# Kernel tuning notes

Measured on AMD Instinct MI355X. Metric: run time of the kernel, lower is better.

Reference implementation:

```python
import jax, jax.numpy as jnp
import numpy as np

B, C, H, W = 2, 256, 64, 64
KEEP = 0.1


def setup_inputs() -> dict:
    key = jax.random.key(0)
    ks = jax.random.split(key, 7)
    s = 0.05  # small init for 1x1-conv weights
    return {
        "x": jax.random.normal(ks[0], (B, C, H, W), dtype=jnp.float32),
        "Wq": jax.random.normal(ks[1], (C, C), dtype=jnp.float32) * s,
        "bq": jax.random.normal(ks[2], (C,), dtype=jnp.float32) * s,
        "Wk": jax.random.normal(ks[3], (C, C), dtype=jnp.float32) * s,
        "bk": jax.random.normal(ks[4], (C,), dtype=jnp.float32) * s,
        "Wv": jax.random.normal(ks[5], (C, C), dtype=jnp.float32) * s,
        "bv": jax.random.normal(ks[6], (C,), dtype=jnp.float32) * s,
    }


def reference(x, Wq, bq, Wk, bk, Wv, bv):
    b, c, h, w = x.shape
    n = h * w

    def proj(Wm, bm):
        # 1x1 conv == per-pixel linear; output as [B, N, C] tokens
        return jnp.einsum('bchw,oc->bhwo', x, Wm).reshape(b, n, c) + bm

    q = proj(Wq, bq)
    k = proj(Wk, bk)
    v = proj(Wv, bv)

    scores = jnp.einsum('bnc,bmc->bnm', q, k) / (c ** 0.5)  # [B, N, N]
    k_keep = max(1, int(KEEP * n))

    vals, idx = jax.lax.top_k(scores, k_keep)  # [B, N, k_keep]
    # softmax over -inf-masked scores == softmax over topk vals scattered into zeros
    probs = jax.nn.softmax(vals, axis=-1)
    attn = jnp.zeros_like(scores).at[
        jnp.arange(b)[:, None, None], jnp.arange(n)[None, :, None], idx
    ].set(probs)

    out = jnp.einsum('bnm,bmc->bnc', attn, v)  # [B, N, C]
    return out.transpose(0, 2, 1).reshape(b, c, h, w)
```

## Files before the change

kernel.cpp:

```cpp
#include <hip/hip_runtime.h>
#include <hip/hip_bf16.h>
#include <math.h>

#define BATCH 2
#define CC    256
#define NN    4096
#define KK    409
#define KCAT  768
#define SCALE 0.0625f
#define PSTRIDE 8192

typedef _Float16 half8 __attribute__((ext_vector_type(8)));
typedef float    floatx4 __attribute__((ext_vector_type(4)));

typedef __attribute__((address_space(3))) unsigned       lds_u32;
typedef __attribute__((address_space(1))) const unsigned glb_u32;
__device__ __forceinline__ void gload16(const void* g, void* l) {
    __builtin_amdgcn_global_load_lds((glb_u32*)g, (lds_u32*)l, 16, 0, 0);
}

__device__ __forceinline__ unsigned fkey(float f) {
    unsigned u = __float_as_uint(f);
    return (u & 0x80000000u) ? ~u : (u | 0x80000000u);
}
__device__ __forceinline__ float keyToF(unsigned k) {
    unsigned u = (k & 0x80000000u) ? (k ^ 0x80000000u) : ~k;
    return __uint_as_float(u);
}

__global__ __launch_bounds__(256) void xpose_wcat_kernel(
        const float* __restrict__ x,
        const float* __restrict__ Wq, const float* __restrict__ Wk,
        const float* __restrict__ Wv,
        _Float16* __restrict__ xcat, _Float16* __restrict__ Wcat) {
    const int t  = threadIdx.x;
    if (blockIdx.y == 4) {
        int idx = (blockIdx.z * 64 + blockIdx.x) * 256 + t;
#pragma unroll
        for (int k = 0; k < 6; k++) {
            int e = idx + k * 32768;
            int mat = e >> 16;
            int o   = (e >> 8) & 255;
            int c   = e & 255;
            const float* W = (mat == 0) ? Wq : (mat == 1) ? Wk : Wv;
            float v = W[o * 256 + c];
            _Float16 hi = (_Float16)v;
            _Float16 lo = (_Float16)(v - (float)hi);
            _Float16* wr = Wcat + ((size_t)(mat * 256 + o)) * KCAT;
            wr[c] = hi; wr[256 + c] = hi; wr[512 + c] = lo;
        }
        return;
    }

    __shared__ float xs[64][68];
    const int n0 = blockIdx.x * 64;
    const int c0 = blockIdx.y * 64;
    const int b  = blockIdx.z;

    {
        const int ci = t >> 2;
        const int j  = (t & 3) * 16;
        const float* xp = x + ((size_t)((b << 8) + c0 + ci)) * NN + n0 + j;
        float4 a0 = ((const float4*)xp)[0];
        float4 a1 = ((const float4*)xp)[1];
        float4 a2 = ((const float4*)xp)[2];
        float4 a3 = ((const float4*)xp)[3];
        *(float4*)&xs[ci][j]      = a0;
        *(float4*)&xs[ci][j + 4]  = a1;
        *(float4*)&xs[ci][j + 8]  = a2;
        *(float4*)&xs[ci][j + 12] = a3;
    }
    __syncthreads();

    const int n = t >> 2;
    const int g0 = t & 3;
    _Float16* xr = xcat + ((size_t)(b * NN + n0 + n)) * KCAT + c0;
#pragma unroll
    for (int gg = 0; gg < 2; gg++) {
        int g = g0 + gg * 4;
        half8 hi, lo;
#pragma unroll
        for (int k = 0; k < 8; k++) {
            float v = xs[g * 8 + k][n];
            _Float16 h = (_Float16)v;
            hi[k] = h;
            lo[k] = (_Float16)(v - (float)h);
        }
        *(half8*)(xr + g * 8)       = hi;
        *(half8*)(xr + 256 + g * 8) = lo;
        *(half8*)(xr + 512 + g * 8) = hi;
    }
}

__global__ __launch_bounds__(256) void proj_gemm(
        const _Float16* __restrict__ xcat, const _Float16* __restrict__ Wcat,
        const float* __restrict__ bq, const float* __restrict__ bk,
        const float* __restrict__ bv,
        _Float16* __restrict__ Qcat, _Float16* __restrict__ Kcat,
        _Float16* __restrict__ Vt) {
    __shared__ _Float16 As[128][64];
    __shared__ _Float16 Bs[128][64];

    const int t    = threadIdx.x;
    const int wave = t >> 6;
    const int l    = t & 63;
    const int wr   = wave >> 1;
    const int wc   = wave & 1;
    const int mat  = blockIdx.z;

    int bym, bxn;
    if (mat < 2) { bym = blockIdx.x >> 1; bxn = blockIdx.x & 1; }
    else         { bym = blockIdx.x & 1;  bxn = blockIdx.x >> 1; }

    const int lr = l >> 3;
    const int gg = (l & 7) ^ lr;

    const _Float16* At;
    const _Float16* Bt;
    if (mat < 2) {
        At = xcat + ((size_t)(bym * 128)) * KCAT;
        Bt = Wcat + ((size_t)(mat * 256 + bxn * 128)) * KCAT;
    } else {
        At = Wcat + ((size_t)(512 + bym * 128)) * KCAT;
        Bt = xcat + ((size_t)(bxn * 128)) * KCAT;
    }
    const size_t lane_off = (size_t)lr * KCAT + gg * 8;

    floatx4 acc[4][4];
#pragma unroll
    for (int i = 0; i < 4; i++)
#pragma unroll
        for (int j = 0; j < 4; j++) acc[i][j] = (floatx4)0.0f;

    const int rowA = l & 15;
    const int sg0  = (l >> 4) ^ (l & 7);
    const int sg1  = sg0 ^ 4;

    for (int kc = 0; kc < KCAT; kc += 64) {
#pragma unroll
        for (int s = 0; s < 4; s++) {
            const int seg = wave * 4 + s;
            gload16(At + (size_t)seg * 8 * KCAT + lane_off + kc, &As[seg * 8][0]);
            gload16(Bt + (size_t)seg * 8 * KCAT + lane_off + kc, &Bs[seg * 8][0]);
        }
        __syncthreads();
#pragma unroll
        for (int ks = 0; ks < 2; ks++) {
            const int sg = ks ? sg1 : sg0;
            half8 af[4], bf[4];
#pragma unroll
            for (int mi = 0; mi < 4; mi++)
                af[mi] = *(const half8*)&As[wr * 64 + mi * 16 + rowA][sg * 8];
#pragma unroll
            for (int ni = 0; ni < 4; ni++)
                bf[ni] = *(const half8*)&Bs[wc * 64 + ni * 16 + rowA][sg * 8];
#pragma unroll
            for (int mi = 0; mi < 4; mi++)
#pragma unroll
                for (int ni = 0; ni < 4; ni++)
                    acc[mi][ni] = __builtin_amdgcn_mfma_f32_16x16x32_f16(
                        af[mi], bf[ni], acc[mi][ni], 0, 0, 0);
        }
        __syncthreads();
    }

    if (mat < 2) {
        const float* bias = (mat == 0) ? bq : bk;
        _Float16* Out = (mat == 0) ? Qcat : Kcat;
#pragma unroll
        for (int ni = 0; ni < 4; ni++) {
            int ch = bxn * 128 + wc * 64 + ni * 16 + (l & 15);
            float bb = bias[ch];
#pragma unroll
            for (int mi = 0; mi < 4; mi++)
#pragma unroll
                for (int rg = 0; rg < 4; rg++) {
                    int token = bym * 128 + wr * 64 + mi * 16 + (l >> 4) * 4 + rg;
                    float v = acc[mi][ni][rg] + bb;
                    _Float16 hi = (_Float16)v;
                    _Float16 lo = (_Float16)(v - (float)hi);
                    _Float16* p = Out + (size_t)token * KCAT + ch;
                    if (mat == 0) { p[0] = hi; p[256] = lo; p[512] = hi; }
                    else          { p[0] = hi; p[256] = hi; p[512] = lo; }
                }
        }
    } else {
#pragma unroll
        for (int mi = 0; mi < 4; mi++)
#pragma unroll
            for (int rg = 0; rg < 4; rg++) {
                int ch = bym * 128 + wr * 64 + mi * 16 + (l >> 4) * 4 + rg;
                float bb = bv[ch];
#pragma unroll
                for (int ni = 0; ni < 4; ni++) {
                    int col = bxn * 128 + wc * 64 + ni * 16 + (l & 15);
                    int b = col >> 12, n = col & 4095;
                    Vt[((size_t)((b << 8) + ch)) * NN + n] =
                        (_Float16)(acc[mi][ni][rg] + bb);
                }
            }
    }
}

__global__ __launch_bounds__(512, 2) void score_gemm(
        const _Float16* __restrict__ Qcat, const _Float16* __restrict__ Kcat,
        float* __restrict__ S) {
    __shared__ _Float16 As[256][64];
    __shared__ _Float16 Bs[256][64];

    const int t    = threadIdx.x;
    const int wave = t >> 6;
    const int l    = t & 63;
    const int wr   = wave >> 1;
    const int wc   = wave & 1;

    const int id  = blockIdx.x;
    const int sc  = id & 7;
    const int j   = id >> 3;
    const int b   = sc & 1;
    const int scq = sc >> 1;
    const int bxn = ((scq & 1) << 3) + (j & 7);
    const int bym = ((scq >> 1) << 3) + (j >> 3);

    const int lr = l >> 3;
    const int gg = (l & 7) ^ lr;

    const _Float16* At = Qcat + ((size_t)((b << 12) + bym * 256)) * KCAT;
    const _Float16* Bt = Kcat + ((size_t)((b << 12) + bxn * 256)) * KCAT;
    const size_t lane_off = (size_t)lr * KCAT + gg * 8;

    floatx4 acc[4][8];
#pragma unroll
    for (int i = 0; i < 4; i++)
#pragma unroll
        for (int jj = 0; jj < 8; jj++) acc[i][jj] = (floatx4)0.0f;

    const int rowA = l & 15;
    const int sg0  = (l >> 4) ^ (l & 7);
    const int sg1  = sg0 ^ 4;

    for (int kc = 0; kc < KCAT; kc += 64) {
#pragma unroll
        for (int s = 0; s < 4; s++) {
            const int seg = wave * 4 + s;
            gload16(At + (size_t)seg * 8 * KCAT + lane_off + kc, &As[seg * 8][0]);
            gload16(Bt + (size_t)seg * 8 * KCAT + lane_off + kc, &Bs[seg * 8][0]);
        }
        __syncthreads();
#pragma unroll
        for (int ks = 0; ks < 2; ks++) {
            const int sg = ks ? sg1 : sg0;
            half8 af[4], bf[8];
#pragma unroll
            for (int mi = 0; mi < 4; mi++)
                af[mi] = *(const half8*)&As[wr * 64 + mi * 16 + rowA][sg * 8];
#pragma unroll
            for (int ni = 0; ni < 8; ni++)
                bf[ni] = *(const half8*)&Bs[wc * 128 + ni * 16 + rowA][sg * 8];
#pragma unroll
            for (int mi = 0; mi < 4; mi++)
#pragma unroll
                for (int ni = 0; ni < 8; ni++)
                    acc[mi][ni] = __builtin_amdgcn_mfma_f32_16x16x32_f16(
                        af[mi], bf[ni], acc[mi][ni], 0, 0, 0);
        }
        __syncthreads();
    }

    float* Sb = S + ((size_t)b << 24);
#pragma unroll
    for (int mi = 0; mi < 4; mi++)
#pragma unroll
        for (int ni = 0; ni < 8; ni++) {
            int col = bxn * 256 + wc * 128 + ni * 16 + (l & 15);
#pragma unroll
            for (int rg = 0; rg < 4; rg++) {
                int row = bym * 256 + wr * 64 + mi * 16 + (l >> 4) * 4 + rg;
                Sb[((size_t)row << 12) + col] = acc[mi][ni][rg] * SCALE;
            }
        }
}

__global__ __launch_bounds__(256) void select_scatter(
        const float* __restrict__ S, _Float16* __restrict__ P) {
    __shared__ unsigned hist[256];
    __shared__ unsigned scan[256];
    __shared__ unsigned candKey[NN];
    __shared__ unsigned wred[4];
    __shared__ float    fmn[4], fmx[4], wsum[4];
    __shared__ unsigned sh_d, sh_cntgt, sh_T;
    __shared__ int      sh_ncand, sh_need;

    const int t = threadIdx.x;
    const int l = t & 63;
    const int w = t >> 6;

    float    val[16];
    unsigned ukey[16];
    {
        const float*  Srow = S + ((size_t)blockIdx.x << 12);
        const float4* sp   = (const float4*)(Srow + t * 16);
#pragma unroll
        for (int jj = 0; jj < 4; jj++) {
            float4 v = sp[jj];
            val[jj * 4 + 0] = v.x; val[jj * 4 + 1] = v.y;
            val[jj * 4 + 2] = v.z; val[jj * 4 + 3] = v.w;
        }
#pragma unroll
        for (int j = 0; j < 16; j++) ukey[j] = fkey(val[j]);
    }

    float lmin = val[0], lmax = val[0];
#pragma unroll
    for (int j = 1; j < 16; j++) {
        lmin = fminf(lmin, val[j]); lmax = fmaxf(lmax, val[j]);
    }
#pragma unroll
    for (int off = 32; off > 0; off >>= 1) {
        float a = __shfl_down(lmin, off);
        float b = __shfl_down(lmax, off);
        if (l + off < 64) { lmin = fminf(lmin, a); lmax = fmaxf(lmax, b); }
    }
    if (l == 0) { fmn[w] = lmin; fmx[w] = lmax; }

    hist[t] = 0u;
    if (t == 0) sh_ncand = 0;
    __syncthreads();
    const float fmin = fminf(fminf(fmn[0], fmn[1]), fminf(fmn[2], fmn[3]));
    const float fmax = fmaxf(fmaxf(fmx[0], fmx[1]), fmaxf(fmx[2], fmx[3]));
    const float range = fmax - fmin;
    const float bscale = (range > 1e-20f) ? 255.0f / range : 0.0f;

    auto binOf = [&](float v) -> int {
        int bin = (int)((v - fmin) * bscale);
        return bin < 0 ? 0 : (bin > 255 ? 255 : bin);
    };

#pragma unroll
    for (int j = 0; j < 16; j++) atomicAdd(&hist[binOf(val[j])], 1u);
    __syncthreads();

    int rem = KK;

    auto find_digit = [&](int remv) {
        unsigned v = hist[t];
#pragma unroll
        for (int off = 1; off < 64; off <<= 1) {
            unsigned o = __shfl_down(v, off);
            if (l + off < 64) v += o;
        }
        if (l == 0) wred[w] = v;
        __syncthreads();
        unsigned add = 0u;
#pragma unroll
        for (int w2 = 0; w2 < 4; w2++) if (w2 > w) add += wred[w2];
        scan[t] = v + add;
        __syncthreads();
        unsigned sufd  = scan[t];
        unsigned sufd1 = (t < 255) ? scan[t + 1] : 0u;
        if (sufd >= (unsigned)remv && sufd1 < (unsigned)remv) {
            sh_d = (unsigned)t; sh_cntgt = sufd1;
        }
        __syncthreads();
    };

    find_digit(rem);
    const int dbin = (int)sh_d;
    rem -= (int)sh_cntgt;

#pragma unroll
    for (int j = 0; j < 16; j++) {
        if (binOf(val[j]) == dbin) {
            int slot = atomicAdd(&sh_ncand, 1);
            candKey[slot] = ukey[j];
        }
    }
    __syncthreads();
    const int nc = sh_ncand;

    if (nc <= 64) {
        if (w == 0) {
            unsigned kl = (l < nc) ? candKey[l] : 0u;
            int r = 0, g = 0;
            for (int j = 0; j < 64; j++) {
                unsigned kj = __shfl(kl, j);
                bool gt = kj > kl;
                g += gt ? 1 : 0;
                r += (gt || (kj == kl && j < l)) ? 1 : 0;
            }
            if (r == rem - 1) { sh_T = kl; sh_need = rem - g; }
        }
    } else {
        unsigned prefix = 0u;
        int rem2 = rem;
        for (int pass = 0; pass < 4; pass++) {
            const int shift = 24 - 8 * pass;
            hist[t] = 0u;
            __syncthreads();
            for (int i = t; i < nc; i += 256) {
                unsigned u2 = candKey[i];
                if (pass == 0 || (u2 >> (shift + 8)) == (prefix >> (shift + 8)))
                    atomicAdd(&hist[(u2 >> shift) & 255u], 1u);
            }
            __syncthreads();
            find_digit(rem2);
            prefix |= (sh_d << shift);
            rem2 -= (int)sh_cntgt;
        }
        if (t == 0) { sh_T = prefix; sh_need = rem2; }
    }
    __syncthreads();
    const unsigned T = sh_T;
    const int need = sh_need;
    const float mT = keyToF(T);

    int eqc = 0;
#pragma unroll
    for (int j = 0; j < 16; j++) if (ukey[j] == T) eqc++;
    int vinc = eqc;
#pragma unroll
    for (int off = 1; off < 64; off <<= 1) {
        int o = __shfl_up(vinc, off);
        if (l >= off) vinc += o;
    }
    if (l == 63) wred[w] = (unsigned)vinc;
    __syncthreads();
    int addlow = 0;
#pragma unroll
    for (int w2 = 0; w2 < 4; w2++) if (w2 < w) addlow += (int)wred[w2];
    const int eqexcl = vinc - eqc + addlow;

    float pv[16];
    float le = 0.f;
#pragma unroll
    for (int j = 0; j < 16; j++) {
        float e = 0.f;
        if (ukey[j] > T) { e = __expf(val[j] - mT); le += e; }
        pv[j] = e;
    }
    if (eqc) {
        int seen = 0;
#pragma unroll
        for (int j = 0; j < 16; j++) {
            if (ukey[j] == T) {
                if (eqexcl + seen < need) { pv[j] = 1.0f; le += 1.0f; }
                seen++;
            }
        }
    }

#pragma unroll
    for (int off = 32; off > 0; off >>= 1) {
        float o = __shfl_down(le, off);
        if (l + off < 64) le += o;
    }
    if (l == 0) wsum[w] = le;
    __syncthreads();
    const float inv = 1.0f / (wsum[0] + wsum[1] + wsum[2] + wsum[3]);

    half8 ra, rb;
#pragma unroll
    for (int j = 0; j < 8; j++) {
        ra[j] = (_Float16)(pv[j] * inv);
        rb[j] = (_Float16)(pv[j + 8] * inv);
    }
    _Float16* Pr = P + (size_t)blockIdx.x * PSTRIDE + t * 16;
    *(half8*)Pr       = ra;
    *(half8*)(Pr + 8) = rb;
}

__global__ __launch_bounds__(256) void av_gemm(
        const _Float16* __restrict__ Vt, const _Float16* __restrict__ P,
        float* __restrict__ out) {
    __shared__ _Float16 As0[64][64], As1[64][64];
    __shared__ _Float16 Bs0[64][64], Bs1[64][64];

    const int t    = threadIdx.x;
    const int wave = t >> 6;
    const int l    = t & 63;
    const int wr   = wave >> 1;
    const int wc   = wave & 1;
    const int bxn  = blockIdx.x;
    const int byc  = blockIdx.y;
    const int b    = blockIdx.z;

    const int lr = l >> 3;
    const int gg = (l & 7) ^ lr;

    const _Float16* At = Vt + ((size_t)((b << 8) + byc * 64)) * NN;
    const _Float16* Bt = P + ((size_t)(b * NN + bxn * 64)) * PSTRIDE;
    const size_t lane_offA = (size_t)lr * NN + gg * 8;
    const size_t lane_offB = (size_t)lr * PSTRIDE + gg * 8;

    floatx4 acc[2][2];
#pragma unroll
    for (int i = 0; i < 2; i++)
#pragma unroll
        for (int j = 0; j < 2; j++) acc[i][j] = (floatx4)0.0f;

    const int rowA   = l & 15;
    const int sgbase = (l >> 4) ^ (l & 7);

    for (int kc = 0; kc < NN; kc += 128) {
#pragma unroll
        for (int s = 0; s < 2; s++) {
            const int seg = wave * 2 + s;
            gload16(At + (size_t)seg * 8 * NN + lane_offA + kc,           &As0[seg * 8][0]);
            gload16(At + (size_t)seg * 8 * NN + lane_offA + kc + 64,      &As1[seg * 8][0]);
            gload16(Bt + (size_t)seg * 8 * PSTRIDE + lane_offB + kc,      &Bs0[seg * 8][0]);
            gload16(Bt + (size_t)seg * 8 * PSTRIDE + lane_offB + kc + 64, &Bs1[seg * 8][0]);
        }
        __syncthreads();
#pragma unroll
        for (int st = 0; st < 4; st++) {
            const _Float16 (*Ap)[64] = (st < 2) ? As0 : As1;
            const _Float16 (*Bp)[64] = (st < 2) ? Bs0 : Bs1;
            const int sg = sgbase ^ ((st & 1) ? 4 : 0);
            half8 af[2], bf[2];
#pragma unroll
            for (int mi = 0; mi < 2; mi++)
                af[mi] = *(const half8*)&Ap[wr * 32 + mi * 16 + rowA][sg * 8];
#pragma unroll
            for (int ni = 0; ni < 2; ni++)
                bf[ni] = *(const half8*)&Bp[wc * 32 + ni * 16 + rowA][sg * 8];
#pragma unroll
            for (int mi = 0; mi < 2; mi++)
#pragma unroll
                for (int ni = 0; ni < 2; ni++)
                    acc[mi][ni] = __builtin_amdgcn_mfma_f32_16x16x32_f16(
                        af[mi], bf[ni], acc[mi][ni], 0, 0, 0);
        }
        __syncthreads();
    }

#pragma unroll
    for (int mi = 0; mi < 2; mi++)
#pragma unroll
        for (int ni = 0; ni < 2; ni++) {
            int col = bxn * 64 + wc * 32 + ni * 16 + (l & 15);
#pragma unroll
            for (int rg = 0; rg < 4; rg++) {
                int row = byc * 64 + wr * 32 + mi * 16 + (l >> 4) * 4 + rg;
                out[((size_t)((b << 8) + row) << 12) + col] = acc[mi][ni][rg];
            }
        }
}

extern "C" void kernel_launch(void* const* d_in, const int* in_sizes, int n_in,
                              void* d_out, int out_size, void* d_ws, size_t ws_size,
                              hipStream_t stream) {
    const float* x  = (const float*)d_in[0];
    const float* Wq = (const float*)d_in[1];
    const float* bq = (const float*)d_in[2];
    const float* Wk = (const float*)d_in[3];
    const float* bk = (const float*)d_in[4];
    const float* Wv = (const float*)d_in[5];
    const float* bv = (const float*)d_in[6];
    float* out = (float*)d_out;

    char* ws = (char*)d_ws;
    _Float16* Wcat = (_Float16*)ws;
    _Float16* Qcat = (_Float16*)(ws + 1179648);
    _Float16* Kcat = (_Float16*)(ws + 1179648 + 12582912);
    _Float16* Vt   = (_Float16*)(ws + 1179648 + 2 * 12582912);
    float*    S    = (float*)   (ws + 1179648 + 2 * 12582912 + 4194304);
    _Float16* xcat = (_Float16*)S;
    _Float16* P    = (_Float16*)S;

    xpose_wcat_kernel<<<dim3(64, 5, BATCH), 256, 0, stream>>>(x, Wq, Wk, Wv,
                                                              xcat, Wcat);
    proj_gemm<<<dim3(128, 1, 3), 256, 0, stream>>>(xcat, Wcat, bq, bk, bv,
                                                   Qcat, Kcat, Vt);
    score_gemm<<<dim3(512, 1, 1), 512, 0, stream>>>(Qcat, Kcat, S);
    select_scatter<<<BATCH * NN, 256, 0, stream>>>(S, P);
    av_gemm<<<dim3(64, 4, BATCH), 256, 0, stream>>>(Vt, P, out);
}
```

Before: 243.7 us.

## Double-buffer score GEMM LDS tiles with prefetch of next K chunk

```diff
diff --git a/kernel.cpp b/kernel.cpp
--- a/kernel.cpp
+++ b/kernel.cpp
@@ -205,8 +205,8 @@
 __global__ __launch_bounds__(512, 2) void score_gemm(
         const _Float16* __restrict__ Qcat, const _Float16* __restrict__ Kcat,
         float* __restrict__ S) {
-    __shared__ _Float16 As[256][64];
-    __shared__ _Float16 Bs[256][64];
+    __shared__ _Float16 As[2][256][32];
+    __shared__ _Float16 Bs[2][256][32];
 
     const int t    = threadIdx.x;
     const int wave = t >> 6;
@@ -222,12 +222,14 @@
     const int bxn = ((scq & 1) << 3) + (j & 7);
     const int bym = ((scq >> 1) << 3) + (j >> 3);
 
-    const int lr = l >> 3;
-    const int gg = (l & 7) ^ lr;
+    const int lr4 = l >> 2;
+    const int gq  = (l & 3) ^ ((l >> 3) & 3);
 
     const _Float16* At = Qcat + ((size_t)((b << 12) + bym * 256)) * KCAT;
     const _Float16* Bt = Kcat + ((size_t)((b << 12) + bxn * 256)) * KCAT;
-    const size_t lane_off = (size_t)lr * KCAT + gg * 8;
+    const size_t lane_off = (size_t)lr4 * KCAT + gq * 8;
+    const size_t segA0 = (size_t)(wave * 2) * 16 * KCAT + lane_off;
+    const size_t segA1 = segA0 + 16 * KCAT;
 
     floatx4 acc[4][8];
 #pragma unroll
@@ -236,35 +238,36 @@
         for (int jj = 0; jj < 8; jj++) acc[i][jj] = (floatx4)0.0f;
 
     const int rowA = l & 15;
-    const int sg0  = (l >> 4) ^ (l & 7);
-    const int sg1  = sg0 ^ 4;
-
-    for (int kc = 0; kc < KCAT; kc += 64) {
-#pragma unroll
-        for (int s = 0; s < 4; s++) {
-            const int seg = wave * 4 + s;
-            gload16(At + (size_t)seg * 8 * KCAT + lane_off + kc, &As[seg * 8][0]);
-            gload16(Bt + (size_t)seg * 8 * KCAT + lane_off + kc, &Bs[seg * 8][0]);
-        }
-        __syncthreads();
-#pragma unroll
-        for (int ks = 0; ks < 2; ks++) {
-            const int sg = ks ? sg1 : sg0;
-            half8 af[4], bf[8];
-#pragma unroll
-            for (int mi = 0; mi < 4; mi++)
-                af[mi] = *(const half8*)&As[wr * 64 + mi * 16 + rowA][sg * 8];
+    const int sg   = (l >> 4) ^ ((l >> 1) & 3);
+
+    gload16(At + segA0, &As[0][wave * 32][0]);
+    gload16(At + segA1, &As[0][wave * 32 + 16][0]);
+    gload16(Bt + segA0, &Bs[0][wave * 32][0]);
+    gload16(Bt + segA1, &Bs[0][wave * 32 + 16][0]);
+
+    for (int it = 0; it < 24; it++) {
+        const int p = it & 1;
+        __syncthreads();
+        if (it + 1 < 24) {
+            const int kc = (it + 1) * 32;
+            gload16(At + segA0 + kc, &As[p ^ 1][wave * 32][0]);
+            gload16(At + segA1 + kc, &As[p ^ 1][wave * 32 + 16][0]);
+            gload16(Bt + segA0 + kc, &Bs[p ^ 1][wave * 32][0]);
+            gload16(Bt + segA1 + kc, &Bs[p ^ 1][wave * 32 + 16][0]);
+        }
+        half8 af[4], bf[8];
+#pragma unroll
+        for (int mi = 0; mi < 4; mi++)
+            af[mi] = *(const half8*)&As[p][wr * 64 + mi * 16 + rowA][sg * 8];
+#pragma unroll
+        for (int ni = 0; ni < 8; ni++)
+            bf[ni] = *(const half8*)&Bs[p][wc * 128 + ni * 16 + rowA][sg * 8];
+#pragma unroll
+        for (int mi = 0; mi < 4; mi++)
 #pragma unroll
             for (int ni = 0; ni < 8; ni++)
-                bf[ni] = *(const half8*)&Bs[wc * 128 + ni * 16 + rowA][sg * 8];
-#pragma unroll
-            for (int mi = 0; mi < 4; mi++)
-#pragma unroll
-                for (int ni = 0; ni < 8; ni++)
-                    acc[mi][ni] = __builtin_amdgcn_mfma_f32_16x16x32_f16(
-                        af[mi], bf[ni], acc[mi][ni], 0, 0, 0);
-        }
-        __syncthreads();
+                acc[mi][ni] = __builtin_amdgcn_mfma_f32_16x16x32_f16(
+                    af[mi], bf[ni], acc[mi][ni], 0, 0, 0);
     }
 
     float* Sb = S + ((size_t)b << 24);
```

Measured after the change: 255.0 us. +4.6%, slower.
